# Kernel optimization log

Hardware: AMD Instinct MI355X
Metric: run time of the kernel (lower is better)

Reference implementation:

```python
import jax, jax.numpy as jnp
import numpy as np

NUM_USERS = 200000
NUM_ITEMS = 100000
NUM_NODES = NUM_USERS + NUM_ITEMS
NUM_EDGES = 600000
DIM = 128
BATCH = 16384


def setup_inputs() -> dict:
    key = jax.random.key(0)
    ks = jax.random.split(key, 7)
    return {
        "user_indices": jax.random.randint(ks[0], (BATCH,), 0, NUM_USERS),
        "item_indices": jax.random.randint(ks[1], (BATCH,), 0, NUM_ITEMS),
        "user_emb": jax.random.normal(ks[2], (NUM_USERS, DIM), jnp.float32) * 0.01,
        "item_emb": jax.random.normal(ks[3], (NUM_ITEMS, DIM), jnp.float32) * 0.01,
        "W": jax.random.normal(ks[4], (DIM, DIM), jnp.float32) * (1.0 / np.sqrt(DIM)),
        "b": jax.random.normal(ks[5], (DIM,), jnp.float32) * 0.01,
        "edge_index": jax.random.randint(ks[6], (2, NUM_EDGES), 0, NUM_NODES),
    }


def reference(user_indices, item_indices, user_emb, item_emb, W, b, edge_index):
    # all node features: [N, D]
    nodes = jnp.concatenate([user_emb, item_emb], axis=0)
    src, dst = edge_index[0], edge_index[1]
    # gather neighbor features [E, D], scatter-add into [N, D]
    agg = jax.ops.segment_sum(nodes[src], dst, num_segments=NUM_NODES)
    # linear transform (nn.Linear: x @ W.T + b)
    prop = agg @ W.T + b
    u = prop[:NUM_USERS][user_indices]   # [B, D]
    i = prop[NUM_USERS:][item_indices]   # [B, D]
    return jnp.sum(u * i, axis=1, keepdims=True)  # [B, 1]
```

## Files before the change

### kernel.cpp

```cpp
#include <hip/hip_runtime.h>

#define NUM_USERS 200000
#define NUM_ITEMS 100000
#define NUM_NODES 300000
#define NUM_EDGES 600000
#define DIM      128
#define BATCH    16384
#define NSLOTS   (2 * BATCH)
#define CAP      32

__global__ void build_map(const int* __restrict__ uidx, const int* __restrict__ iidx,
                          int* __restrict__ map) {
    int t = blockIdx.x * 256 + threadIdx.x;
    if (t >= NSLOTS) return;
    int node = (t < BATCH) ? uidx[t] : (NUM_USERS + iidx[t - BATCH]);
    atomicCAS(&map[node], -1, t);
}

__global__ void bin_edges(const int* __restrict__ edges, const int* __restrict__ map,
                          int* __restrict__ cnt, int* __restrict__ bucket) {
    int e = blockIdx.x * 256 + threadIdx.x;
    if (e >= NUM_EDGES) return;
    int dst = edges[NUM_EDGES + e];
    int s = map[dst];
    if (s < 0) return;
    int src = edges[e];
    int p = atomicAdd(&cnt[s], 1);
    if (p < CAP) bucket[s * CAP + p] = src;
}

__global__ __launch_bounds__(256) void gather(const int* __restrict__ cnt,
                                              const int* __restrict__ bucket,
                                              const float* __restrict__ uemb,
                                              const float* __restrict__ iemb,
                                              float* __restrict__ agg) {
    int s = blockIdx.x * 4 + (threadIdx.x >> 6);
    int lane = threadIdx.x & 63;
    int n = cnt[s]; if (n > CAP) n = CAP;
    const int* bk = bucket + s * CAP;

    float2 v[4];
#pragma unroll
    for (int k = 0; k < 4; ++k) {
        int src = bk[k];
        if (src < 0 || src >= NUM_NODES) src = 0;
        const float* row = (src < NUM_USERS)
            ? uemb + (size_t)src * DIM
            : iemb + (size_t)(src - NUM_USERS) * DIM;
        v[k] = ((const float2*)row)[lane];
    }
    float2 acc = {0.f, 0.f};
#pragma unroll
    for (int k = 0; k < 4; ++k)
        if (k < n) { acc.x += v[k].x; acc.y += v[k].y; }
    for (int k = 4; k < n; ++k) {
        int src = bk[k];
        const float* row = (src < NUM_USERS)
            ? uemb + (size_t)src * DIM
            : iemb + (size_t)(src - NUM_USERS) * DIM;
        float2 t = ((const float2*)row)[lane];
        acc.x += t.x; acc.y += t.y;
    }
    ((float2*)(agg + (size_t)s * DIM))[lane] = acc;
}

#define SPB 32
__global__ __launch_bounds__(256) void transform(const float* __restrict__ agg,
                                                 const float* __restrict__ W,
                                                 const float* __restrict__ bias,
                                                 float* __restrict__ prop) {
    __shared__ float4 lds[SPB * DIM / 4];
    int base = blockIdx.x * SPB;
    int tid = threadIdx.x;

    const float4* ag = (const float4*)(agg + (size_t)base * DIM);
#pragma unroll
    for (int i = 0; i < SPB * DIM / 4 / 256; ++i)
        lds[i * 256 + tid] = ag[i * 256 + tid];

    int j = tid & 127;
    int half = tid >> 7;
    float4 wj[DIM / 4];
    const float4* wrow = (const float4*)(W + j * DIM);
#pragma unroll
    for (int kk = 0; kk < DIM / 4; ++kk) wj[kk] = wrow[kk];
    float bj = bias[j];
    __syncthreads();

#pragma unroll
    for (int g = 0; g < 4; ++g) {
        int s0 = half * 16 + g * 4;
        const float4* a0 = lds + (s0 + 0) * (DIM / 4);
        const float4* a1 = lds + (s0 + 1) * (DIM / 4);
        const float4* a2 = lds + (s0 + 2) * (DIM / 4);
        const float4* a3 = lds + (s0 + 3) * (DIM / 4);
        float c0 = bj, c1 = bj, c2 = bj, c3 = bj;
#pragma unroll
        for (int kk = 0; kk < DIM / 4; ++kk) {
            float4 w4 = wj[kk];
            float4 x0 = a0[kk], x1 = a1[kk], x2 = a2[kk], x3 = a3[kk];
            c0 += x0.x * w4.x + x0.y * w4.y + x0.z * w4.z + x0.w * w4.w;
            c1 += x1.x * w4.x + x1.y * w4.y + x1.z * w4.z + x1.w * w4.w;
            c2 += x2.x * w4.x + x2.y * w4.y + x2.z * w4.z + x2.w * w4.w;
            c3 += x3.x * w4.x + x3.y * w4.y + x3.z * w4.z + x3.w * w4.w;
        }
        prop[(size_t)(base + s0 + 0) * DIM + j] = c0;
        prop[(size_t)(base + s0 + 1) * DIM + j] = c1;
        prop[(size_t)(base + s0 + 2) * DIM + j] = c2;
        prop[(size_t)(base + s0 + 3) * DIM + j] = c3;
    }
}

__global__ void final_dot(const int* __restrict__ uidx, const int* __restrict__ iidx,
                          const int* __restrict__ map, const float* __restrict__ prop,
                          float* __restrict__ out) {
    int o = blockIdx.x * 4 + (threadIdx.x >> 6);
    if (o >= BATCH) return;
    int lane = threadIdx.x & 63;
    int su = map[uidx[o]];
    int si = map[NUM_USERS + iidx[o]];
    float2 a = ((const float2*)(prop + (size_t)su * DIM))[lane];
    float2 c = ((const float2*)(prop + (size_t)si * DIM))[lane];
    float v = a.x * c.x + a.y * c.y;
#pragma unroll
    for (int off = 32; off > 0; off >>= 1) v += __shfl_down(v, off);
    if (lane == 0) out[o] = v;
}

extern "C" void kernel_launch(void* const* d_in, const int* in_sizes, int n_in,
                              void* d_out, int out_size, void* d_ws, size_t ws_size,
                              hipStream_t stream) {
    const int*   uidx  = (const int*)d_in[0];
    const int*   iidx  = (const int*)d_in[1];
    const float* uemb  = (const float*)d_in[2];
    const float* iemb  = (const float*)d_in[3];
    const float* W     = (const float*)d_in[4];
    const float* bias  = (const float*)d_in[5];
    const int*   edges = (const int*)d_in[6];
    float*       out   = (float*)d_out;

    char* ws = (char*)d_ws;
    int*   map    = (int*)ws;
    int*   cnt    = (int*)(ws + (2u << 20));
    int*   bucket = (int*)(ws + (3u << 20));
    float* agg    = (float*)(ws + (8u << 20));
    float* prop   = (float*)(ws + (8u << 20) + (size_t)NSLOTS * DIM * 4);

    hipMemsetAsync(map, 0xFF, NUM_NODES * sizeof(int), stream);
    hipMemsetAsync(cnt, 0, NSLOTS * sizeof(int), stream);

    build_map<<<(NSLOTS + 255) / 256, 256, 0, stream>>>(uidx, iidx, map);
    bin_edges<<<(NUM_EDGES + 255) / 256, 256, 0, stream>>>(edges, map, cnt, bucket);
    gather<<<NSLOTS / 4, 256, 0, stream>>>(cnt, bucket, uemb, iemb, agg);
    transform<<<NSLOTS / SPB, 256, 0, stream>>>(agg, W, bias, prop);
    final_dot<<<(BATCH + 3) / 4, 256, 0, stream>>>(uidx, iidx, map, prop, out);
}
```

Baseline: 238.2 us.

## Run the linear transform on bf16 MFMA and store aggregates in bf16

Replaces the scalar FP32 LDS-based matrix transform with a kernel that uses the 16x16x32 bf16 MFMA instruction. Aggregated node rows are rounded to bf16 in the gather kernel, and W is converted to bf16 by a new small kernel. The aim is to cut transform compute time and halve the traffic for the intermediate buffer, at the cost of bf16 rounding error and one extra kernel launch.

```diff
diff --git a/kernel.cpp b/kernel.cpp
--- a/kernel.cpp
+++ b/kernel.cpp
@@ -8,6 +8,21 @@
 #define BATCH    16384
 #define NSLOTS   (2 * BATCH)
 #define CAP      32
+
+typedef __attribute__((ext_vector_type(4))) float f32x4;
+typedef __attribute__((ext_vector_type(8))) short bf16x8;
+
+static __device__ __forceinline__ ushort f2bf(float x) {
+    unsigned u = __float_as_uint(x);
+    return (ushort)((u + 0x7FFF + ((u >> 16) & 1)) >> 16);
+}
+
+__global__ void wconv(const float* __restrict__ W, ushort* __restrict__ Wb) {
+    int t = blockIdx.x * 256 + threadIdx.x;
+    float4 v = ((const float4*)W)[t];
+    ushort4 o = { f2bf(v.x), f2bf(v.y), f2bf(v.z), f2bf(v.w) };
+    ((ushort4*)Wb)[t] = o;
+}
 
 __global__ void build_map(const int* __restrict__ uidx, const int* __restrict__ iidx,
                           int* __restrict__ map) {
@@ -33,7 +48,7 @@
                                               const int* __restrict__ bucket,
                                               const float* __restrict__ uemb,
                                               const float* __restrict__ iemb,
-                                              float* __restrict__ agg) {
+                                              ushort* __restrict__ aggb) {
     int s = blockIdx.x * 4 + (threadIdx.x >> 6);
     int lane = threadIdx.x & 63;
     int n = cnt[s]; if (n > CAP) n = CAP;
@@ -61,53 +76,38 @@
         float2 t = ((const float2*)row)[lane];
         acc.x += t.x; acc.y += t.y;
     }
-    ((float2*)(agg + (size_t)s * DIM))[lane] = acc;
+    ushort2 ob = { f2bf(acc.x), f2bf(acc.y) };
+    ((ushort2*)(aggb + (size_t)s * DIM))[lane] = ob;
 }
 
-#define SPB 32
-__global__ __launch_bounds__(256) void transform(const float* __restrict__ agg,
-                                                 const float* __restrict__ W,
-                                                 const float* __restrict__ bias,
-                                                 float* __restrict__ prop) {
-    __shared__ float4 lds[SPB * DIM / 4];
-    int base = blockIdx.x * SPB;
-    int tid = threadIdx.x;
+__global__ __launch_bounds__(256) void transform_mfma(
+        const ushort* __restrict__ aggb, const ushort* __restrict__ Wb,
+        const float* __restrict__ bias, float* __restrict__ prop) {
+    int wave = threadIdx.x >> 6, lane = threadIdx.x & 63;
+    int lr = lane & 15, lg = lane >> 4;
+    int s0 = blockIdx.x * 64 + wave * 16;
 
-    const float4* ag = (const float4*)(agg + (size_t)base * DIM);
+    f32x4 acc[8];
 #pragma unroll
-    for (int i = 0; i < SPB * DIM / 4 / 256; ++i)
-        lds[i * 256 + tid] = ag[i * 256 + tid];
+    for (int jt = 0; jt < 8; ++jt) acc[jt] = (f32x4){0.f, 0.f, 0.f, 0.f};
 
-    int j = tid & 127;
-    int half = tid >> 7;
-    float4 wj[DIM / 4];
-    const float4* wrow = (const float4*)(W + j * DIM);
+    const ushort* pa = aggb + (size_t)(s0 + lr) * DIM + lg * 8;
+    const ushort* pw = Wb + lr * DIM + lg * 8;
 #pragma unroll
-    for (int kk = 0; kk < DIM / 4; ++kk) wj[kk] = wrow[kk];
-    float bj = bias[j];
-    __syncthreads();
-
+    for (int ks = 0; ks < 4; ++ks) {
+        bf16x8 af = *(const bf16x8*)(pa + ks * 32);
 #pragma unroll
-    for (int g = 0; g < 4; ++g) {
-        int s0 = half * 16 + g * 4;
-        const float4* a0 = lds + (s0 + 0) * (DIM / 4);
-        const float4* a1 = lds + (s0 + 1) * (DIM / 4);
-        const float4* a2 = lds + (s0 + 2) * (DIM / 4);
-        const float4* a3 = lds + (s0 + 3) * (DIM / 4);
-        float c0 = bj, c1 = bj, c2 = bj, c3 = bj;
+        for (int jt = 0; jt < 8; ++jt) {
+            bf16x8 wf = *(const bf16x8*)(pw + jt * 16 * DIM + ks * 32);
+            acc[jt] = __builtin_amdgcn_mfma_f32_16x16x32_bf16(af, wf, acc[jt], 0, 0, 0);
+        }
+    }
 #pragma unroll
-        for (int kk = 0; kk < DIM / 4; ++kk) {
-            float4 w4 = wj[kk];
-            float4 x0 = a0[kk], x1 = a1[kk], x2 = a2[kk], x3 = a3[kk];
-            c0 += x0.x * w4.x + x0.y * w4.y + x0.z * w4.z + x0.w * w4.w;
-            c1 += x1.x * w4.x + x1.y * w4.y + x1.z * w4.z + x1.w * w4.w;
-            c2 += x2.x * w4.x + x2.y * w4.y + x2.z * w4.z + x2.w * w4.w;
-            c3 += x3.x * w4.x + x3.y * w4.y + x3.z * w4.z + x3.w * w4.w;
-        }
-        prop[(size_t)(base + s0 + 0) * DIM + j] = c0;
-        prop[(size_t)(base + s0 + 1) * DIM + j] = c1;
-        prop[(size_t)(base + s0 + 2) * DIM + j] = c2;
-        prop[(size_t)(base + s0 + 3) * DIM + j] = c3;
+    for (int jt = 0; jt < 8; ++jt) {
+        float bj = bias[jt * 16 + lr];
+#pragma unroll
+        for (int r = 0; r < 4; ++r)
+            prop[(size_t)(s0 + lg * 4 + r) * DIM + jt * 16 + lr] = acc[jt][r] + bj;
     }
 }
 
@@ -140,18 +140,20 @@
     float*       out   = (float*)d_out;
 
     char* ws = (char*)d_ws;
-    int*   map    = (int*)ws;
-    int*   cnt    = (int*)(ws + (2u << 20));
-    int*   bucket = (int*)(ws + (3u << 20));
-    float* agg    = (float*)(ws + (8u << 20));
-    float* prop   = (float*)(ws + (8u << 20) + (size_t)NSLOTS * DIM * 4);
+    int*    map    = (int*)ws;
+    int*    cnt    = (int*)(ws + (2u << 20));
+    int*    bucket = (int*)(ws + (3u << 20));
+    ushort* Wb     = (ushort*)(ws + (7u << 20));
+    ushort* aggb   = (ushort*)(ws + (8u << 20));
+    float*  prop   = (float*)(ws + (16u << 20));
 
     hipMemsetAsync(map, 0xFF, NUM_NODES * sizeof(int), stream);
     hipMemsetAsync(cnt, 0, NSLOTS * sizeof(int), stream);
 
+    wconv<<<16, 256, 0, stream>>>(W, Wb);
     build_map<<<(NSLOTS + 255) / 256, 256, 0, stream>>>(uidx, iidx, map);
     bin_edges<<<(NUM_EDGES + 255) / 256, 256, 0, stream>>>(edges, map, cnt, bucket);
-    gather<<<NSLOTS / 4, 256, 0, stream>>>(cnt, bucket, uemb, iemb, agg);
-    transform<<<NSLOTS / SPB, 256, 0, stream>>>(agg, W, bias, prop);
+    gather<<<NSLOTS / 4, 256, 0, stream>>>(cnt, bucket, uemb, iemb, aggb);
+    transform_mfma<<<NSLOTS / 64, 256, 0, stream>>>(aggb, Wb, bias, prop);
     final_dot<<<(BATCH + 3) / 4, 256, 0, stream>>>(uidx, iidx, map, prop, out);
 }
```

Result: faster. 213.8 us (-10.2%).
